# Kernel tuning notes

Measured on AMD Instinct MI355X. Metric: run time of the kernel, lower is better.

The kernel has to match this reference:

```python
import jax, jax.numpy as jnp
import numpy as np

B, T = 256, 64
EMBED, GRU, HID = 1024, 1024, 1024
SD, SC = 32, 32
ADIM = 6
UNIMIX = 0.01
SFLAT = SD * SC


def setup_inputs() -> dict:
    key = jax.random.key(0)
    ks = jax.random.split(key, 16)
    rn = lambda k, s: jax.random.normal(k, s, jnp.float32) * 0.02
    return {
        "embeds": jax.random.normal(ks[0], (B, T, EMBED), jnp.float32),
        "actions": jax.random.uniform(ks[1], (B, T, ADIM), jnp.float32),
        "h_init": jnp.zeros((B, GRU), jnp.float32),
        "z_init": jnp.zeros((B, SD, SC), jnp.float32),
        "W_pre": rn(ks[2], (HID, SFLAT + ADIM)), "b_pre": jnp.zeros((HID,)),
        "g_pre": jnp.ones((HID,)), "be_pre": jnp.zeros((HID,)),
        "W_ih": rn(ks[3], (3 * GRU, HID)), "W_hh": rn(ks[4], (3 * GRU, GRU)),
        "b_ih": jnp.zeros((3 * GRU,)), "b_hh": jnp.zeros((3 * GRU,)),
        "g_gn": jnp.ones((GRU,)), "b_gn": jnp.zeros((GRU,)),
        "Wp1": rn(ks[5], (HID, GRU)), "bp1": jnp.zeros((HID,)),
        "gp": jnp.ones((HID,)), "bpn": jnp.zeros((HID,)),
        "Wp2": rn(ks[6], (SFLAT, HID)), "bp2": jnp.zeros((SFLAT,)),
        "Wq1": rn(ks[7], (HID, GRU + EMBED)), "bq1": jnp.zeros((HID,)),
        "gq": jnp.ones((HID,)), "bqn": jnp.zeros((HID,)),
        "Wq2": rn(ks[8], (SFLAT, HID)), "bq2": jnp.zeros((SFLAT,)),
        # pre-drawn uniform noise -> gumbel, for categorical sampling per step
        "u_prior": jax.random.uniform(ks[9], (T, B, SD, SC), jnp.float32, 1e-6, 1.0 - 1e-6),
        "u_post": jax.random.uniform(ks[10], (T, B, SD, SC), jnp.float32, 1e-6, 1.0 - 1e-6),
    }


def _ln(x, g, b, eps=1e-5):
    m = jnp.mean(x, -1, keepdims=True)
    v = jnp.var(x, -1, keepdims=True)
    return (x - m) * jax.lax.rsqrt(v + eps) * g + b


def _mlp(x, W1, b1, g, bn, W2, b2):
    h = jax.nn.silu(_ln(x @ W1.T + b1, g, bn))
    return h @ W2.T + b2


def _sample(logits, u):
    # logits: (B, SD*SC), u: (B, SD, SC) uniform noise
    lg = logits.reshape(logits.shape[0], SD, SC)
    probs = jax.nn.softmax(lg, axis=-1)
    probs = (1.0 - UNIMIX) * probs + UNIMIX / SC
    gumbel = -jnp.log(-jnp.log(u))
    idx = jnp.argmax(jnp.log(probs) + gumbel, axis=-1)  # multinomial sample
    oh = jax.nn.one_hot(idx, SC, dtype=probs.dtype)
    z = oh + probs - jax.lax.stop_gradient(probs)  # straight-through
    return z, probs


def reference(embeds, actions, h_init, z_init,
              W_pre, b_pre, g_pre, be_pre,
              W_ih, W_hh, b_ih, b_hh, g_gn, b_gn,
              Wp1, bp1, gp, bpn, Wp2, bp2,
              Wq1, bq1, gq, bqn, Wq2, bq2,
              u_prior, u_post):
    def step(carry, xs):
        h, z = carry
        a, e, up, uq = xs
        x = jnp.concatenate([z.reshape(z.shape[0], -1), a], axis=-1)
        x = jax.nn.silu(_ln(x @ W_pre.T + b_pre, g_pre, be_pre))
        # GRUCell
        gx = x @ W_ih.T + b_ih
        gh = h @ W_hh.T + b_hh
        xr, xu, xn = jnp.split(gx, 3, axis=-1)
        hr, hu, hn = jnp.split(gh, 3, axis=-1)
        r = jax.nn.sigmoid(xr + hr)
        u_gate = jax.nn.sigmoid(xu + hu)
        n = jnp.tanh(xn + r * hn)
        h = (1.0 - u_gate) * n + u_gate * h
        h = _ln(h, g_gn, b_gn)
        prior_logits = _mlp(h, Wp1, bp1, gp, bpn, Wp2, bp2)
        _, prior_p = _sample(prior_logits, up)
        post_logits = _mlp(jnp.concatenate([h, e], axis=-1), Wq1, bq1, gq, bqn, Wq2, bq2)
        post_z, post_p = _sample(post_logits, uq)
        return (h, post_z), (h, post_z, prior_p, post_p)

    xs = (jnp.swapaxes(actions, 0, 1), jnp.swapaxes(embeds, 0, 1), u_prior, u_post)
    _, (hs, zs, pp, qp) = jax.lax.scan(step, (h_init, z_init), xs)
    # (T,B,...) -> (B,T,...)
    return (jnp.swapaxes(hs, 0, 1), jnp.swapaxes(zs, 0, 1),
            jnp.swapaxes(pp, 0, 1), jnp.swapaxes(qp, 0, 1))
```

## Files before the change

### kernel.cpp

```cpp
#include <hip/hip_runtime.h>
#include <hip/hip_bf16.h>
#include <math.h>


struct GArg {
  const float* A0; int lda0;
  const float* A1; int lda1;
  int kSplit;
  const float* W; int ldw;
  float* C; int N; int K;
};

struct LArg {
  const float* Y; int S;
  const float* bias; const float* g; const float* be;
  float* O;
};

__device__ __forceinline__ float exp_cr(float x)  { return (float)exp((double)x); }
__device__ __forceinline__ float log_cr(float x)  { return (float)log((double)x); }
__device__ __forceinline__ float tanh_cr(float x) { return (float)tanh((double)x); }
__device__ __forceinline__ float sigmoid_cr(float x) {
  float e = exp_cr(-x);
  float d = __fadd_rn(1.0f, e);
  return __fdiv_rn(1.0f, d);
}

__global__ __launch_bounds__(256) void gemm_k(GArg g0, GArg g1, GArg g2,
                                              int z1, int z2) {
  int z = blockIdx.z;
  GArg G; int s;
  if (z < z1)      { G = g0; s = z; }
  else if (z < z2) { G = g1; s = z - z1; }
  else             { G = g2; s = z - z2; }
  int n0 = blockIdx.x * 64;
  if (n0 >= G.N) return;
  int m0 = blockIdx.y * 64;

  __shared__ float As[2][16][68];
  __shared__ float Bs[2][16][68];

  int tid = threadIdx.x;
  int tx = tid & 15, ty = tid >> 4;
  int kq = tid & 3,  rr = tid >> 2;

  bool vecOK = ((G.ldw & 3) == 0) && ((G.lda0 & 3) == 0) && ((G.lda1 & 3) == 0)
            && (((G.kSplit & 15) == 0) || (G.kSplit >= G.K));

  float acc[4][4];
  #pragma unroll
  for (int j = 0; j < 4; ++j)
    #pragma unroll
    for (int i = 0; i < 4; ++i) acc[j][i] = 0.0f;

  int nt = (G.K + 15) >> 4;
  int t0 = s * 24, t1 = min(nt, t0 + 24);

  float a[4], w[4];
  int useVec = 0;

  auto stage_load = [&](int kt) {
    int kb = kt * 16;
    useVec = vecOK && (kb + 16 <= G.K);
    if (useVec) {
      int k = kb + kq * 4;
      float4 av = (k < G.kSplit)
        ? *(const float4*)(G.A0 + (size_t)(m0 + rr) * G.lda0 + k)
        : *(const float4*)(G.A1 + (size_t)(m0 + rr) * G.lda1 + (k - G.kSplit));
      float4 wv = *(const float4*)(G.W + (size_t)(n0 + rr) * G.ldw + k);
      a[0] = av.x; a[1] = av.y; a[2] = av.z; a[3] = av.w;
      w[0] = wv.x; w[1] = wv.y; w[2] = wv.z; w[3] = wv.w;
    } else {
      int k = kb + tx;
      #pragma unroll
      for (int i = 0; i < 4; ++i) { a[i] = 0.0f; w[i] = 0.0f; }
      if (k < G.K) {
        if (k < G.kSplit) {
          const float* Ap = G.A0 + (size_t)(m0 + ty * 4) * G.lda0 + k;
          #pragma unroll
          for (int i = 0; i < 4; ++i) a[i] = Ap[(size_t)i * G.lda0];
        } else {
          const float* Ap = G.A1 + (size_t)(m0 + ty * 4) * G.lda1 + (k - G.kSplit);
          #pragma unroll
          for (int i = 0; i < 4; ++i) a[i] = Ap[(size_t)i * G.lda1];
        }
        const float* Wp = G.W + (size_t)(n0 + ty * 4) * G.ldw + k;
        #pragma unroll
        for (int i = 0; i < 4; ++i) w[i] = Wp[(size_t)i * G.ldw];
      }
    }
  };
  auto stage_write = [&](int b) {
    if (useVec) {
      #pragma unroll
      for (int i = 0; i < 4; ++i) {
        As[b][kq * 4 + i][rr] = a[i];
        Bs[b][kq * 4 + i][rr] = w[i];
      }
    } else {
      *(float4*)&As[b][tx][ty * 4] = make_float4(a[0], a[1], a[2], a[3]);
      *(float4*)&Bs[b][tx][ty * 4] = make_float4(w[0], w[1], w[2], w[3]);
    }
  };
  auto compute = [&](int b) {
    #pragma unroll
    for (int kk = 0; kk < 16; ++kk) {
      float4 av = *(const float4*)&As[b][kk][ty * 4];
      float4 bv = *(const float4*)&Bs[b][kk][tx * 4];
      float aa[4] = {av.x, av.y, av.z, av.w};
      float bb[4] = {bv.x, bv.y, bv.z, bv.w};
      #pragma unroll
      for (int j = 0; j < 4; ++j)
        #pragma unroll
        for (int i = 0; i < 4; ++i)
          acc[j][i] = fmaf(aa[j], bb[i], acc[j][i]);
    }
  };

  stage_load(t0); stage_write(0); __syncthreads();
  int cur = 0;
  for (int kt = t0; kt < t1; ++kt) {
    if (kt + 1 < t1) {
      stage_load(kt + 1);
      compute(cur);
      stage_write(cur ^ 1);
      __syncthreads();
      cur ^= 1;
    } else compute(cur);
  }

  float* Cp = G.C + (size_t)s * 256 * G.N;
  #pragma unroll
  for (int j = 0; j < 4; ++j)
    *(float4*)&Cp[(size_t)(m0 + ty * 4 + j) * G.N + n0 + tx * 4] =
      make_float4(acc[j][0], acc[j][1], acc[j][2], acc[j][3]);
}

__global__ __launch_bounds__(256) void lnsilu2_k(LArg l0, LArg l1) {
  LArg L = blockIdx.y ? l1 : l0;
  __shared__ float xs[64][20];
  __shared__ float stats[2];
  int row = blockIdx.x, tid = threadIdx.x;
  int cl = tid & 63, iq = tid >> 6;
  int kb = cl >> 3, j = cl & 7;

  float xv[4];
  #pragma unroll
  for (int q = 0; q < 4; ++q) {
    int i = iq * 4 + q;
    int n = kb * 128 + 8 * i + j;
    size_t idx = (size_t)row * 1024 + n;
    float x = L.Y[idx];
    for (int ss = 1; ss < L.S; ++ss) x = __fadd_rn(x, L.Y[(size_t)ss * 262144 + idx]);
    x = __fadd_rn(x, L.bias[n]);
    xv[q] = x;
    xs[cl][i] = x;
  }
  __syncthreads();
  if (tid < 64) {
    float r = xs[cl][0];
    #pragma unroll
    for (int i = 1; i < 16; ++i) r = __fadd_rn(r, xs[cl][i]);
    r = __fadd_rn(r, __shfl_xor(r, 1));
    r = __fadd_rn(r, __shfl_xor(r, 2));
    r = __fadd_rn(r, __shfl_xor(r, 4));
    r = __fadd_rn(r, __shfl_xor(r, 8));
    r = __fadd_rn(r, __shfl_xor(r, 16));
    r = __fadd_rn(r, __shfl_xor(r, 32));
    float mean = __fmul_rn(r, 0.0009765625f);
    float d0 = __fsub_rn(xs[cl][0], mean);
    float r2 = __fmul_rn(d0, d0);
    #pragma unroll
    for (int i = 1; i < 16; ++i) {
      float d = __fsub_rn(xs[cl][i], mean);
      r2 = __fadd_rn(r2, __fmul_rn(d, d));
    }
    r2 = __fadd_rn(r2, __shfl_xor(r2, 1));
    r2 = __fadd_rn(r2, __shfl_xor(r2, 2));
    r2 = __fadd_rn(r2, __shfl_xor(r2, 4));
    r2 = __fadd_rn(r2, __shfl_xor(r2, 8));
    r2 = __fadd_rn(r2, __shfl_xor(r2, 16));
    r2 = __fadd_rn(r2, __shfl_xor(r2, 32));
    float var = __fmul_rn(r2, 0.0009765625f);
    float sdv = __fsqrt_rn(__fadd_rn(var, (float)1e-5));
    if (cl == 0) { stats[0] = mean; stats[1] = __fdiv_rn(1.0f, sdv); }
  }
  __syncthreads();
  float mean = stats[0], rstd = stats[1];
  #pragma unroll
  for (int q = 0; q < 4; ++q) {
    int i = iq * 4 + q;
    int n = kb * 128 + 8 * i + j;
    float d = __fsub_rn(xv[q], mean);
    float t = __fmul_rn(__fmul_rn(d, rstd), L.g[n]);
    t = __fadd_rn(t, L.be[n]);
    L.O[(size_t)row * 1024 + n] = __fmul_rn(t, sigmoid_cr(t));
  }
}

__global__ __launch_bounds__(256) void gru256_k(
  const float* GX, const float* GH, float* H,
  const float* b_ih, const float* b_hh, const float* g_gn, const float* b_gn,
  float* out, int t)
{
  __shared__ float xs[64][20];
  __shared__ float stats[2];
  int row = blockIdx.x, tid = threadIdx.x;
  int cl = tid & 63, iq = tid >> 6;
  int kb = cl >> 3, j = cl & 7;

  float hv[4];
  #pragma unroll
  for (int q = 0; q < 4; ++q) {
    int i = iq * 4 + q;
    int n = kb * 128 + 8 * i + j;
    size_t i0 = (size_t)row * 3072 + n;
    #define FOLD3(P, off) __fadd_rn(__fadd_rn((P)[off], (P)[786432 + (off)]), (P)[1572864 + (off)])
    float xr = __fadd_rn(FOLD3(GX, i0),        b_ih[n]);
    float xu = __fadd_rn(FOLD3(GX, i0 + 1024), b_ih[n + 1024]);
    float xn = __fadd_rn(FOLD3(GX, i0 + 2048), b_ih[n + 2048]);
    float hr = __fadd_rn(FOLD3(GH, i0),        b_hh[n]);
    float hu = __fadd_rn(FOLD3(GH, i0 + 1024), b_hh[n + 1024]);
    float hn = __fadd_rn(FOLD3(GH, i0 + 2048), b_hh[n + 2048]);
    #undef FOLD3
    float r = sigmoid_cr(__fadd_rn(xr, hr));
    float u = sigmoid_cr(__fadd_rn(xu, hu));
    float nn = tanh_cr(__fadd_rn(xn, __fmul_rn(r, hn)));
    float h2 = __fadd_rn(__fmul_rn(__fsub_rn(1.0f, u), nn),
                         __fmul_rn(u, H[(size_t)row * 1024 + n]));
    hv[q] = h2;
    xs[cl][i] = h2;
  }
  __syncthreads();
  if (tid < 64) {
    float r = xs[cl][0];
    #pragma unroll
    for (int i = 1; i < 16; ++i) r = __fadd_rn(r, xs[cl][i]);
    r = __fadd_rn(r, __shfl_xor(r, 1));
    r = __fadd_rn(r, __shfl_xor(r, 2));
    r = __fadd_rn(r, __shfl_xor(r, 4));
    r = __fadd_rn(r, __shfl_xor(r, 8));
    r = __fadd_rn(r, __shfl_xor(r, 16));
    r = __fadd_rn(r, __shfl_xor(r, 32));
    float mean = __fmul_rn(r, 0.0009765625f);
    float d0 = __fsub_rn(xs[cl][0], mean);
    float r2 = __fmul_rn(d0, d0);
    #pragma unroll
    for (int i = 1; i < 16; ++i) {
      float d = __fsub_rn(xs[cl][i], mean);
      r2 = __fadd_rn(r2, __fmul_rn(d, d));
    }
    r2 = __fadd_rn(r2, __shfl_xor(r2, 1));
    r2 = __fadd_rn(r2, __shfl_xor(r2, 2));
    r2 = __fadd_rn(r2, __shfl_xor(r2, 4));
    r2 = __fadd_rn(r2, __shfl_xor(r2, 8));
    r2 = __fadd_rn(r2, __shfl_xor(r2, 16));
    r2 = __fadd_rn(r2, __shfl_xor(r2, 32));
    float var = __fmul_rn(r2, 0.0009765625f);
    float sdv = __fsqrt_rn(__fadd_rn(var, (float)1e-5));
    if (cl == 0) { stats[0] = mean; stats[1] = __fdiv_rn(1.0f, sdv); }
  }
  __syncthreads();
  float mean = stats[0], rstd = stats[1];
  #pragma unroll
  for (int q = 0; q < 4; ++q) {
    int i = iq * 4 + q;
    int n = kb * 128 + 8 * i + j;
    float d = __fsub_rn(hv[q], mean);
    float h3 = __fadd_rn(__fmul_rn(__fmul_rn(d, rstd), g_gn[n]), b_gn[n]);
    H[(size_t)row * 1024 + n] = h3;
    out[((size_t)row * 64 + t) * 1024 + n] = h3;
  }
}

__global__ __launch_bounds__(256) void fused_k(
  const float* Yq, const float* bq2, const float* Y2p, const float* bp2,
  const float* u_post, const float* actions,
  const float* W_pre, const float* b_pre, const float* g_pre, const float* be_pre,
  float* XPRE, float* out, int t)
{
  const size_t NOUT = 16777216ull;
  __shared__ int   sidx[32];
  __shared__ float szval[32];
  __shared__ float sact[8];
  __shared__ float xs[64][20];
  __shared__ float stats[2];
  int b = blockIdx.x, tid = threadIdx.x;
  int d = tid >> 3, lane = tid & 7;
  const float C0 = (float)(1.0 - 0.01);
  const float C1 = (float)(0.01 / 32.0);
  size_t ob = ((size_t)b * 64 + t) * 1024;

  {
    float lg[4];
    #pragma unroll
    for (int i = 0; i < 4; ++i) {
      int col = d * 32 + lane + 8 * i;
      size_t idx = (size_t)b * 1024 + col;
      float x = __fadd_rn(__fadd_rn(Yq[idx], Yq[262144 + idx]), Yq[524288 + idx]);
      lg[i] = __fadd_rn(x, bq2[col]);
    }
    float mx = fmaxf(fmaxf(lg[0], lg[1]), fmaxf(lg[2], lg[3]));
    for (int off = 4; off; off >>= 1) mx = fmaxf(mx, __shfl_xor(mx, off, 8));
    float e[4];
    #pragma unroll
    for (int i = 0; i < 4; ++i) e[i] = exp_cr(__fsub_rn(lg[i], mx));
    float ssum = e[0];
    ssum = __fadd_rn(ssum, e[1]);
    ssum = __fadd_rn(ssum, e[2]);
    ssum = __fadd_rn(ssum, e[3]);
    ssum = __fadd_rn(ssum, __shfl_xor(ssum, 1, 8));
    ssum = __fadd_rn(ssum, __shfl_xor(ssum, 2, 8));
    ssum = __fadd_rn(ssum, __shfl_xor(ssum, 4, 8));
    float p[4];
    #pragma unroll
    for (int i = 0; i < 4; ++i) {
      float pr = __fdiv_rn(e[i], ssum);
      p[i] = __fadd_rn(__fmul_rn(C0, pr), C1);
    }
    float bv = -3.4e38f; int bc = 33;
    #pragma unroll
    for (int i = 0; i < 4; ++i) {
      int c = lane + 8 * i, col = d * 32 + c;
      out[3 * NOUT + ob + col] = p[i];
      float uu = u_post[((size_t)t * 256 + b) * 1024 + col];
      float l1 = log_cr(uu);
      float v1 = -l1;
      float l2 = log_cr(v1);
      float gu = -l2;
      float lp = log_cr(p[i]);
      float val = __fadd_rn(lp, gu);
      if (val > bv) { bv = val; bc = c; }
    }
    for (int off = 4; off; off >>= 1) {
      float ov = __shfl_xor(bv, off, 8);
      int   oc = __shfl_xor(bc, off, 8);
      if (ov > bv || (ov == bv && oc < bc)) { bv = ov; bc = oc; }
    }
    #pragma unroll
    for (int i = 0; i < 4; ++i) {
      int c = lane + 8 * i, col = d * 32 + c;
      float zv = 0.0f;
      if (c == bc) { zv = __fsub_rn(__fadd_rn(1.0f, p[i]), p[i]); szval[d] = zv; }
      out[NOUT + ob + col] = zv;
    }
    if (lane == 0) sidx[d] = bc;
  }

  {
    float lg[4];
    #pragma unroll
    for (int i = 0; i < 4; ++i) {
      int col = d * 32 + lane + 8 * i;
      size_t idx = (size_t)b * 1024 + col;
      float x = __fadd_rn(__fadd_rn(Y2p[idx], Y2p[262144 + idx]), Y2p[524288 + idx]);
      lg[i] = __fadd_rn(x, bp2[col]);
    }
    float mx = fmaxf(fmaxf(lg[0], lg[1]), fmaxf(lg[2], lg[3]));
    for (int off = 4; off; off >>= 1) mx = fmaxf(mx, __shfl_xor(mx, off, 8));
    float e[4];
    #pragma unroll
    for (int i = 0; i < 4; ++i) e[i] = exp_cr(__fsub_rn(lg[i], mx));
    float ssum = e[0];
    ssum = __fadd_rn(ssum, e[1]);
    ssum = __fadd_rn(ssum, e[2]);
    ssum = __fadd_rn(ssum, e[3]);
    ssum = __fadd_rn(ssum, __shfl_xor(ssum, 1, 8));
    ssum = __fadd_rn(ssum, __shfl_xor(ssum, 2, 8));
    ssum = __fadd_rn(ssum, __shfl_xor(ssum, 4, 8));
    #pragma unroll
    for (int i = 0; i < 4; ++i) {
      int col = d * 32 + lane + 8 * i;
      float pr = __fdiv_rn(e[i], ssum);
      out[2 * NOUT + ob + col] = __fadd_rn(__fmul_rn(C0, pr), C1);
    }
  }

  if (t < 63) {
    if (tid < 6) sact[tid] = actions[((size_t)b * 64 + (t + 1)) * 6 + tid];
    __syncthreads();
    int cl = tid & 63, iq = tid >> 6;
    int kb = cl >> 3, j = cl & 7;
    float xv[4];
    #pragma unroll
    for (int q = 0; q < 4; ++q) {
      int i = iq * 4 + q;
      int n = kb * 128 + 8 * i + j;
      const float* Wr = W_pre + (size_t)n * 1030;
      float p0 = 0.0f, p1 = 0.0f, p2 = 0.0f;
      #pragma unroll
      for (int dd = 0; dd < 12; ++dd)
        p0 = fmaf(szval[dd], Wr[dd * 32 + sidx[dd]], p0);
      #pragma unroll
      for (int dd = 12; dd < 24; ++dd)
        p1 = fmaf(szval[dd], Wr[dd * 32 + sidx[dd]], p1);
      #pragma unroll
      for (int dd = 24; dd < 32; ++dd)
        p2 = fmaf(szval[dd], Wr[dd * 32 + sidx[dd]], p2);
      #pragma unroll
      for (int ai = 0; ai < 6; ++ai)
        p2 = fmaf(sact[ai], Wr[1024 + ai], p2);
      float x = __fadd_rn(__fadd_rn(p0, p1), p2);
      x = __fadd_rn(x, b_pre[n]);
      xv[q] = x;
      xs[cl][i] = x;
    }
    __syncthreads();
    if (tid < 64) {
      float r = xs[cl][0];
      #pragma unroll
      for (int i = 1; i < 16; ++i) r = __fadd_rn(r, xs[cl][i]);
      r = __fadd_rn(r, __shfl_xor(r, 1));
      r = __fadd_rn(r, __shfl_xor(r, 2));
      r = __fadd_rn(r, __shfl_xor(r, 4));
      r = __fadd_rn(r, __shfl_xor(r, 8));
      r = __fadd_rn(r, __shfl_xor(r, 16));
      r = __fadd_rn(r, __shfl_xor(r, 32));
      float mean = __fmul_rn(r, 0.0009765625f);
      float d0 = __fsub_rn(xs[cl][0], mean);
      float r2 = __fmul_rn(d0, d0);
      #pragma unroll
      for (int i = 1; i < 16; ++i) {
        float dd = __fsub_rn(xs[cl][i], mean);
        r2 = __fadd_rn(r2, __fmul_rn(dd, dd));
      }
      r2 = __fadd_rn(r2, __shfl_xor(r2, 1));
      r2 = __fadd_rn(r2, __shfl_xor(r2, 2));
      r2 = __fadd_rn(r2, __shfl_xor(r2, 4));
      r2 = __fadd_rn(r2, __shfl_xor(r2, 8));
      r2 = __fadd_rn(r2, __shfl_xor(r2, 16));
      r2 = __fadd_rn(r2, __shfl_xor(r2, 32));
      float var = __fmul_rn(r2, 0.0009765625f);
      float sdv = __fsqrt_rn(__fadd_rn(var, (float)1e-5));
      if (cl == 0) { stats[0] = mean; stats[1] = __fdiv_rn(1.0f, sdv); }
    }
    __syncthreads();
    float mean = stats[0], rstd = stats[1];
    #pragma unroll
    for (int q = 0; q < 4; ++q) {
      int i = iq * 4 + q;
      int n = kb * 128 + 8 * i + j;
      float dd = __fsub_rn(xv[q], mean);
      float tt = __fmul_rn(__fmul_rn(dd, rstd), g_pre[n]);
      tt = __fadd_rn(tt, be_pre[n]);
      XPRE[(size_t)b * 1024 + n] = __fmul_rn(tt, sigmoid_cr(tt));
    }
  }
}

__global__ __launch_bounds__(256) void init_k(const float* h_init, const float* z_init,
                                              const float* actions, float* H, float* XZ)
{
  int b = blockIdx.x, tid = threadIdx.x;
  #pragma unroll
  for (int j = 0; j < 4; ++j) {
    int n = tid + j * 256;
    H [(size_t)b * 1024 + n] = h_init[(size_t)b * 1024 + n];
    XZ[(size_t)b * 1040 + n] = z_init[(size_t)b * 1024 + n];
  }
  if (tid < 6) XZ[(size_t)b * 1040 + 1024 + tid] = actions[(size_t)b * 64 * 6 + tid];
}

extern "C" void kernel_launch(void* const* d_in, const int* in_sizes, int n_in,
                              void* d_out, int out_size, void* d_ws, size_t ws_size,
                              hipStream_t stream)
{
  const float* embeds  = (const float*)d_in[0];
  const float* actions = (const float*)d_in[1];
  const float* h_init  = (const float*)d_in[2];
  const float* z_init  = (const float*)d_in[3];
  const float* W_pre   = (const float*)d_in[4];
  const float* b_pre   = (const float*)d_in[5];
  const float* g_pre   = (const float*)d_in[6];
  const float* be_pre  = (const float*)d_in[7];
  const float* W_ih    = (const float*)d_in[8];
  const float* W_hh    = (const float*)d_in[9];
  const float* b_ih    = (const float*)d_in[10];
  const float* b_hh    = (const float*)d_in[11];
  const float* g_gn    = (const float*)d_in[12];
  const float* b_gn    = (const float*)d_in[13];
  const float* Wp1     = (const float*)d_in[14];
  const float* bp1     = (const float*)d_in[15];
  const float* gp      = (const float*)d_in[16];
  const float* bpn     = (const float*)d_in[17];
  const float* Wp2     = (const float*)d_in[18];
  const float* bp2     = (const float*)d_in[19];
  const float* Wq1     = (const float*)d_in[20];
  const float* bq1     = (const float*)d_in[21];
  const float* gq      = (const float*)d_in[22];
  const float* bqn     = (const float*)d_in[23];
  const float* Wq2     = (const float*)d_in[24];
  const float* bq2     = (const float*)d_in[25];
  const float* u_post  = (const float*)d_in[27];
  float* out           = (float*)d_out;
  const int KS = 1 << 30;

  float* W0   = (float*)d_ws;
  float* H    = W0;
  float* XZ   = W0 + 262144;
  float* PREY = W0 + 528384;
  float* Q1A  = PREY;
  float* GX   = W0 + 1314816;
  float* GH   = W0 + 3674112;
  float* YQ   = W0 + 6033408;
  float* Y2p  = YQ;
  float* YQ2  = W0 + 7606272;
  float* XPRE = YQ2;
  float* Y1p  = W0 + 8392704;
  float* P1Ap = W0 + 9179136;

  hipLaunchKernelGGL(init_k, dim3(256), dim3(256), 0, stream, h_init, z_init, actions, H, XZ);

  GArg pre0{XZ, 1040, XZ, 1040, KS, W_pre, 1030, PREY, 1024, 1030};
  hipLaunchKernelGGL(gemm_k, dim3(16, 4, 3), dim3(256), 0, stream, pre0, pre0, pre0, 3, 3);
  {
    LArg lp{PREY, 3, b_pre, g_pre, be_pre, XPRE};
    hipLaunchKernelGGL(lnsilu2_k, dim3(256, 1), dim3(256), 0, stream, lp, lp);
    GArg gx{XPRE, 1024, XPRE, 1024, KS, W_ih, 1024, GX, 3072, 1024};
    GArg gh{H,    1024, H,    1024, KS, W_hh, 1024, GH, 3072, 1024};
    hipLaunchKernelGGL(gemm_k, dim3(48, 4, 6), dim3(256), 0, stream, gx, gh, gh, 3, 6);
  }

  for (int t = 0; t < 64; ++t) {
    hipLaunchKernelGGL(gru256_k, dim3(256), dim3(256), 0, stream,
                       GX, GH, H, b_ih, b_hh, g_gn, b_gn, out, t);
    GArg q1 {H, 1024, embeds + (size_t)t * 1024, 65536, 1024, Wq1, 2048, YQ, 1024, 2048};
    GArg gh {H, 1024, H, 1024, KS, W_hh, 1024, GH, 3072, 1024};
    GArg py1{out + (size_t)t * 1024, 65536, out, 65536, KS, Wp1, 1024, Y1p, 1024, 1024};
    if (t < 63)
      hipLaunchKernelGGL(gemm_k, dim3(48, 4, 12), dim3(256), 0, stream, q1, gh, py1, 6, 9);
    else
      hipLaunchKernelGGL(gemm_k, dim3(48, 4, 9), dim3(256), 0, stream, q1, q1, py1, 6, 6);
    {
      LArg lq{YQ, 6, bq1, gq, bqn, Q1A};
      LArg lr{Y1p, 3, bp1, gp, bpn, P1Ap};
      hipLaunchKernelGGL(lnsilu2_k, dim3(256, 2), dim3(256), 0, stream, lq, lr);
    }
    GArg q2 {Q1A,  1024, Q1A,  1024, KS, Wq2, 1024, YQ2, 1024, 1024};
    GArg py2{P1Ap, 1024, P1Ap, 1024, KS, Wp2, 1024, Y2p, 1024, 1024};
    hipLaunchKernelGGL(gemm_k, dim3(16, 4, 6), dim3(256), 0, stream, q2, q2, py2, 3, 3);
    hipLaunchKernelGGL(fused_k, dim3(256), dim3(256), 0, stream,
                       YQ2, bq2, Y2p, bp2, u_post, actions,
                       W_pre, b_pre, g_pre, be_pre, XPRE, out, t);
    if (t < 63) {
      GArg gx{XPRE, 1024, XPRE, 1024, KS, W_ih, 1024, GX, 3072, 1024};
      hipLaunchKernelGGL(gemm_k, dim3(48, 4, 3), dim3(256), 0, stream, gx, gx, gx, 3, 3);
    }
  }
}
```

Baseline: 11.56 ms.

## Flatten GEMM grid to avoid idle blocks and transpose W_pre for coalesced gathers

The GEMM launch switches from a 3D grid, where blocks with n0 beyond N exited early, to a flat 1D grid whose block index is decoded into sub-problem, split-K slice and tile. This removes idle blocks when problems of different N share one launch. A one-time transpose of the z-part of W_pre is added so fused_k's per-step one-hot gather reads contiguous columns across threads rather than strided rows. The workspace layout is reshuffled so the transposed weights reuse the XZ scratch area, and the split-K decode now relies on N being a multiple of 64.

```diff
diff --git a/kernel.cpp b/kernel.cpp
--- a/kernel.cpp
+++ b/kernel.cpp
@@ -27,15 +27,18 @@
 }
 
 __global__ __launch_bounds__(256) void gemm_k(GArg g0, GArg g1, GArg g2,
-                                              int z1, int z2) {
-  int z = blockIdx.z;
-  GArg G; int s;
-  if (z < z1)      { G = g0; s = z; }
-  else if (z < z2) { G = g1; s = z - z1; }
-  else             { G = g2; s = z - z2; }
-  int n0 = blockIdx.x * 64;
-  if (n0 >= G.N) return;
-  int m0 = blockIdx.y * 64;
+                                              int c0, int c01) {
+  int l = blockIdx.x;
+  GArg G;
+  if (l < c0)       { G = g0; }
+  else if (l < c01) { G = g1; l -= c0; }
+  else              { G = g2; l -= c01; }
+  int nbx = G.N >> 6;
+  int per = nbx * 4;
+  int s   = l / per;
+  int rem = l % per;
+  int m0  = (rem / nbx) * 64;
+  int n0  = (rem % nbx) * 64;
 
   __shared__ float As[2][16][68];
   __shared__ float Bs[2][16][68];
@@ -273,10 +276,21 @@
   }
 }
 
+__global__ __launch_bounds__(256) void trans_k(const float* W_pre, float* W_preT)
+{
+  int k = blockIdx.x, tid = threadIdx.x;
+  #pragma unroll
+  for (int q = 0; q < 4; ++q) {
+    int n = tid + q * 256;
+    W_preT[(size_t)k * 1024 + n] = W_pre[(size_t)n * 1030 + k];
+  }
+}
+
 __global__ __launch_bounds__(256) void fused_k(
   const float* Yq, const float* bq2, const float* Y2p, const float* bp2,
   const float* u_post, const float* actions,
-  const float* W_pre, const float* b_pre, const float* g_pre, const float* be_pre,
+  const float* W_pre, const float* W_preT,
+  const float* b_pre, const float* g_pre, const float* be_pre,
   float* XPRE, float* out, int t)
 {
   const size_t NOUT = 16777216ull;
@@ -386,17 +400,17 @@
     for (int q = 0; q < 4; ++q) {
       int i = iq * 4 + q;
       int n = kb * 128 + 8 * i + j;
+      float p0 = 0.0f, p1 = 0.0f, p2 = 0.0f;
+      #pragma unroll
+      for (int dd = 0; dd < 12; ++dd)
+        p0 = fmaf(szval[dd], W_preT[(size_t)(dd * 32 + sidx[dd]) * 1024 + n], p0);
+      #pragma unroll
+      for (int dd = 12; dd < 24; ++dd)
+        p1 = fmaf(szval[dd], W_preT[(size_t)(dd * 32 + sidx[dd]) * 1024 + n], p1);
+      #pragma unroll
+      for (int dd = 24; dd < 32; ++dd)
+        p2 = fmaf(szval[dd], W_preT[(size_t)(dd * 32 + sidx[dd]) * 1024 + n], p2);
       const float* Wr = W_pre + (size_t)n * 1030;
-      float p0 = 0.0f, p1 = 0.0f, p2 = 0.0f;
-      #pragma unroll
-      for (int dd = 0; dd < 12; ++dd)
-        p0 = fmaf(szval[dd], Wr[dd * 32 + sidx[dd]], p0);
-      #pragma unroll
-      for (int dd = 12; dd < 24; ++dd)
-        p1 = fmaf(szval[dd], Wr[dd * 32 + sidx[dd]], p1);
-      #pragma unroll
-      for (int dd = 24; dd < 32; ++dd)
-        p2 = fmaf(szval[dd], Wr[dd * 32 + sidx[dd]], p2);
       #pragma unroll
       for (int ai = 0; ai < 6; ++ai)
         p2 = fmaf(sact[ai], Wr[1024 + ai], p2);
@@ -497,29 +511,31 @@
 
   float* W0   = (float*)d_ws;
   float* H    = W0;
-  float* XZ   = W0 + 262144;
-  float* PREY = W0 + 528384;
-  float* Q1A  = PREY;
-  float* GX   = W0 + 1314816;
-  float* GH   = W0 + 3674112;
-  float* YQ   = W0 + 6033408;
+  float* Q1A  = W0 + 262144;
+  float* GX   = W0 + 524288;
+  float* GH   = W0 + 2883584;
+  float* YQ   = W0 + 5242880;
   float* Y2p  = YQ;
-  float* YQ2  = W0 + 7606272;
+  float* PREY = YQ;
+  float* YQ2  = W0 + 6815744;
   float* XPRE = YQ2;
-  float* Y1p  = W0 + 8392704;
-  float* P1Ap = W0 + 9179136;
+  float* Y1p  = W0 + 7602176;
+  float* P1Ap = W0 + 8388608;
+  float* WpT  = W0 + 8650752;
+  float* XZ   = WpT;
 
   hipLaunchKernelGGL(init_k, dim3(256), dim3(256), 0, stream, h_init, z_init, actions, H, XZ);
 
   GArg pre0{XZ, 1040, XZ, 1040, KS, W_pre, 1030, PREY, 1024, 1030};
-  hipLaunchKernelGGL(gemm_k, dim3(16, 4, 3), dim3(256), 0, stream, pre0, pre0, pre0, 3, 3);
+  hipLaunchKernelGGL(gemm_k, dim3(192), dim3(256), 0, stream, pre0, pre0, pre0, 192, 192);
   {
     LArg lp{PREY, 3, b_pre, g_pre, be_pre, XPRE};
     hipLaunchKernelGGL(lnsilu2_k, dim3(256, 1), dim3(256), 0, stream, lp, lp);
     GArg gx{XPRE, 1024, XPRE, 1024, KS, W_ih, 1024, GX, 3072, 1024};
     GArg gh{H,    1024, H,    1024, KS, W_hh, 1024, GH, 3072, 1024};
-    hipLaunchKernelGGL(gemm_k, dim3(48, 4, 6), dim3(256), 0, stream, gx, gh, gh, 3, 6);
-  }
+    hipLaunchKernelGGL(gemm_k, dim3(1152), dim3(256), 0, stream, gx, gh, gh, 576, 1152);
+  }
+  hipLaunchKernelGGL(trans_k, dim3(1024), dim3(256), 0, stream, W_pre, WpT);
 
   for (int t = 0; t < 64; ++t) {
     hipLaunchKernelGGL(gru256_k, dim3(256), dim3(256), 0, stream,
@@ -528,9 +544,9 @@
     GArg gh {H, 1024, H, 1024, KS, W_hh, 1024, GH, 3072, 1024};
     GArg py1{out + (size_t)t * 1024, 65536, out, 65536, KS, Wp1, 1024, Y1p, 1024, 1024};
     if (t < 63)
-      hipLaunchKernelGGL(gemm_k, dim3(48, 4, 12), dim3(256), 0, stream, q1, gh, py1, 6, 9);
+      hipLaunchKernelGGL(gemm_k, dim3(1152), dim3(256), 0, stream, q1, gh, py1, 384, 960);
     else
-      hipLaunchKernelGGL(gemm_k, dim3(48, 4, 9), dim3(256), 0, stream, q1, q1, py1, 6, 6);
+      hipLaunchKernelGGL(gemm_k, dim3(576), dim3(256), 0, stream, q1, q1, py1, 384, 384);
     {
       LArg lq{YQ, 6, bq1, gq, bqn, Q1A};
       LArg lr{Y1p, 3, bp1, gp, bpn, P1Ap};
@@ -538,13 +554,13 @@
     }
     GArg q2 {Q1A,  1024, Q1A,  1024, KS, Wq2, 1024, YQ2, 1024, 1024};
     GArg py2{P1Ap, 1024, P1Ap, 1024, KS, Wp2, 1024, Y2p, 1024, 1024};
-    hipLaunchKernelGGL(gemm_k, dim3(16, 4, 6), dim3(256), 0, stream, q2, q2, py2, 3, 3);
+    hipLaunchKernelGGL(gemm_k, dim3(384), dim3(256), 0, stream, q2, py2, py2, 192, 384);
     hipLaunchKernelGGL(fused_k, dim3(256), dim3(256), 0, stream,
                        YQ2, bq2, Y2p, bp2, u_post, actions,
-                       W_pre, b_pre, g_pre, be_pre, XPRE, out, t);
+                       W_pre, WpT, b_pre, g_pre, be_pre, XPRE, out, t);
     if (t < 63) {
       GArg gx{XPRE, 1024, XPRE, 1024, KS, W_ih, 1024, GX, 3072, 1024};
-      hipLaunchKernelGGL(gemm_k, dim3(48, 4, 3), dim3(256), 0, stream, gx, gx, gx, 3, 3);
-    }
-  }
-}
+      hipLaunchKernelGGL(gemm_k, dim3(576), dim3(256), 0, stream, gx, gx, gx, 576, 576);
+    }
+  }
+}
```

After: 9.616 ms, median of 2. 1.2x faster.
